# Performance work log

Measured on AMD Instinct MI355X. Metric: run time of the kernel, lower is better.

The kernel has to match this reference:

```python
import jax, jax.numpy as jnp
import numpy as np

D_MODEL = 1024
N_HEADS = 16
HEAD_DIM = D_MODEL // N_HEADS
D_FF = 4 * D_MODEL
B, T = 2, 2048
EPS = 1e-5


def setup_inputs() -> dict:
    key = jax.random.key(0)
    ks = jax.random.split(key, 12)
    s = 0.02
    x = jax.random.normal(ks[0], (B, T, D_MODEL), dtype=jnp.float32)
    # causal mask: True where attention is disallowed (masked_fill semantics)
    mask = jnp.triu(jnp.ones((T, T), dtype=bool), k=1)[None, None]
    def lin(k, out_d, in_d):
        return jax.random.normal(k, (out_d, in_d), dtype=jnp.float32) * s
    return {
        "x": x,
        "mask": mask,
        "wq_w": lin(ks[1], D_MODEL, D_MODEL), "wq_b": jnp.zeros((D_MODEL,), jnp.float32),
        "wk_w": lin(ks[2], D_MODEL, D_MODEL), "wk_b": jnp.zeros((D_MODEL,), jnp.float32),
        "wv_w": lin(ks[3], D_MODEL, D_MODEL), "wv_b": jnp.zeros((D_MODEL,), jnp.float32),
        "wo_w": lin(ks[4], D_MODEL, D_MODEL), "wo_b": jnp.zeros((D_MODEL,), jnp.float32),
        "fc1_w": lin(ks[5], D_FF, D_MODEL), "fc1_b": jnp.zeros((D_FF,), jnp.float32),
        "fc2_w": lin(ks[6], D_MODEL, D_FF), "fc2_b": jnp.zeros((D_MODEL,), jnp.float32),
        "ln1_g": jnp.ones((D_MODEL,), jnp.float32), "ln1_b": jnp.zeros((D_MODEL,), jnp.float32),
        "ln2_g": jnp.ones((D_MODEL,), jnp.float32), "ln2_b": jnp.zeros((D_MODEL,), jnp.float32),
    }


def _layer_norm(x, g, b):
    mu = jnp.mean(x, axis=-1, keepdims=True)
    var = jnp.mean(jnp.square(x - mu), axis=-1, keepdims=True)
    return (x - mu) * jax.lax.rsqrt(var + EPS) * g + b


def reference(x, mask, wq_w, wq_b, wk_w, wk_b, wv_w, wv_b, wo_w, wo_b,
              fc1_w, fc1_b, fc2_w, fc2_b, ln1_g, ln1_b, ln2_g, ln2_b):
    Bx, Tx, C = x.shape
    # --- attention sub-block (pre-norm) ---
    h = _layer_norm(x, ln1_g, ln1_b)
    q = h @ wq_w.T + wq_b
    k = h @ wk_w.T + wk_b
    v = h @ wv_w.T + wv_b
    # split heads: [B,T,C] -> [B,H,T,Dh]
    def split(t):
        return t.reshape(Bx, Tx, N_HEADS, HEAD_DIM).transpose(0, 2, 1, 3)
    q, k, v = split(q), split(k), split(v)
    scores = jnp.einsum('bhqd,bhkd->bhqk', q, k) / jnp.sqrt(jnp.float32(HEAD_DIM))
    scores = jnp.where(mask, jnp.float32(-1e9), scores)
    attn = jax.nn.softmax(scores, axis=-1)
    ctx = jnp.einsum('bhqk,bhkd->bhqd', attn, v)
    ctx = ctx.transpose(0, 2, 1, 3).reshape(Bx, Tx, C)
    x = x + (ctx @ wo_w.T + wo_b)
    # --- FFN sub-block (pre-norm) ---
    h = _layer_norm(x, ln2_g, ln2_b)
    h = jax.nn.gelu(h @ fc1_w.T + fc1_b, approximate=False)
    x = x + (h @ fc2_w.T + fc2_b)
    return x
```

## Files before the change

### kernel.cpp

```cpp
#include <hip/hip_runtime.h>
#include <stdint.h>

typedef unsigned short u16;
typedef __bf16 bf16x8 __attribute__((ext_vector_type(8)));
typedef float floatx4 __attribute__((ext_vector_type(4)));

#define AS1(p) ((__attribute__((address_space(1))) void*)(void*)(p))
#define AS3(p) ((__attribute__((address_space(3))) void*)(p))

__device__ __forceinline__ u16 f2bf(float f) {
    unsigned u;
    __builtin_memcpy(&u, &f, 4);
    u += 0x7FFF + ((u >> 16) & 1);
    return (u16)(u >> 16);
}
__device__ __forceinline__ u16 f2bf_trunc(float f) {
    unsigned u;
    __builtin_memcpy(&u, &f, 4);
    return (u16)(u >> 16);
}
__device__ __forceinline__ float exp2_fast(float x) {
    return __builtin_amdgcn_exp2f(x);
}
__device__ __forceinline__ float gelu_f(float x) {
    return 0.5f * x * (1.0f + erff(x * 0.70710678118654752f));
}

__global__ __launch_bounds__(256) void conv_w_kernel(
    const float* __restrict__ wq, const float* __restrict__ wk,
    const float* __restrict__ wv, const float* __restrict__ wo,
    const float* __restrict__ f1, const float* __restrict__ f2,
    const float* __restrict__ bq, const float* __restrict__ bk,
    const float* __restrict__ bv, float* __restrict__ qkvb,
    u16* __restrict__ W) {
    const size_t i4 = ((size_t)blockIdx.x * 256 + threadIdx.x) * 4;
    const size_t M1 = 1048576;
    const float* src;
    size_t off;
    if (i4 < M1)            { src = wq; off = i4; }
    else if (i4 < 2 * M1)   { src = wk; off = i4 - M1; }
    else if (i4 < 3 * M1)   { src = wv; off = i4 - 2 * M1; }
    else if (i4 < 4 * M1)   { src = wo; off = i4 - 3 * M1; }
    else if (i4 < 8 * M1)   { src = f1; off = i4 - 4 * M1; }
    else                    { src = f2; off = i4 - 8 * M1; }
    float4 d = *(const float4*)(src + off);
    ushort4 o;
    o.x = f2bf(d.x); o.y = f2bf(d.y); o.z = f2bf(d.z); o.w = f2bf(d.w);
    *(ushort4*)(W + i4) = o;
    if (blockIdx.x == 0) {
        for (int i = threadIdx.x; i < 1024; i += 256) {
            qkvb[i] = bq[i];
            qkvb[1024 + i] = bk[i];
            qkvb[2048 + i] = bv[i];
        }
    }
}

__global__ __launch_bounds__(64) void ln_kernel(const float* __restrict__ X,
                                                const float* __restrict__ G,
                                                const float* __restrict__ Bt,
                                                u16* __restrict__ Y) {
    const int row = blockIdx.x;
    const int lane = threadIdx.x;
    const float* xr = X + (size_t)row * 1024;
    float v[16];
    float s = 0.f;
#pragma unroll
    for (int i = 0; i < 16; ++i) { v[i] = xr[lane + i * 64]; s += v[i]; }
#pragma unroll
    for (int off = 1; off < 64; off <<= 1) s += __shfl_xor(s, off, 64);
    const float mu = s * (1.0f / 1024.0f);
    float ss = 0.f;
#pragma unroll
    for (int i = 0; i < 16; ++i) { float d = v[i] - mu; ss += d * d; }
#pragma unroll
    for (int off = 1; off < 64; off <<= 1) ss += __shfl_xor(ss, off, 64);
    const float rstd = rsqrtf(ss * (1.0f / 1024.0f) + 1e-5f);
    u16* yr = Y + (size_t)row * 1024;
#pragma unroll
    for (int i = 0; i < 16; ++i) {
        int c = lane + i * 64;
        yr[c] = f2bf((v[i] - mu) * rstd * G[c] + Bt[c]);
    }
}

template <int BM>
__global__ __launch_bounds__(256) void gemm_kernel(
    const u16* __restrict__ A, const u16* __restrict__ Bt,
    const float* __restrict__ bias, const float* __restrict__ resid,
    void* __restrict__ Cp, int M, int N, int K, int act, int c_f32) {
    constexpr int NI = BM / 32;
    __shared__ __align__(16) u16 lA[BM * 64];
    __shared__ __align__(16) u16 lB[128 * 64];
    const int tid = threadIdx.x;
    const int wave = tid >> 6, lane = tid & 63;
    const int wm = (wave >> 1) * (BM / 2), wn = (wave & 1) * 64;
    const int lr = lane & 15, lk8 = (lane >> 4) * 8;
    int bid = blockIdx.y * gridDim.x + blockIdx.x;
    { const int nwg = gridDim.x * gridDim.y;
      const int q = nwg >> 3, r = nwg & 7, xcd = bid & 7, lid = bid >> 3;
      bid = (xcd < r ? xcd * (q + 1) : r * (q + 1) + (xcd - r) * q) + lid; }
    const int m0 = (bid % gridDim.x) * BM, n0 = (bid / gridDim.x) * 128;
    const int srow = tid >> 3, scol = (tid & 7) * 8;

    floatx4 acc[NI][4];
#pragma unroll
    for (int i = 0; i < NI; ++i)
#pragma unroll
        for (int j = 0; j < 4; ++j) acc[i][j] = floatx4{0.f, 0.f, 0.f, 0.f};

    const u16* Ab = A + (size_t)m0 * K;
    const u16* Bb = Bt + (size_t)n0 * K;

    for (int k0 = 0; k0 < K; k0 += 64) {
#pragma unroll
        for (int r = 0; r < BM / 32; ++r) {
            int row = srow + r * 32;
            __builtin_amdgcn_global_load_lds(AS1(Ab + (size_t)row * K + k0 + scol),
                                             AS3(lA + row * 64 + scol), 16, 0, 0);
        }
#pragma unroll
        for (int r = 0; r < 4; ++r) {
            int row = srow + r * 32;
            __builtin_amdgcn_global_load_lds(AS1(Bb + (size_t)row * K + k0 + scol),
                                             AS3(lB + row * 64 + scol), 16, 0, 0);
        }
        __syncthreads();
#pragma unroll
        for (int kk = 0; kk < 64; kk += 32) {
            bf16x8 af[NI], bfr[4];
#pragma unroll
            for (int i = 0; i < NI; ++i)
                af[i] = *(const bf16x8*)&lA[(wm + i * 16 + lr) * 64 + kk + lk8];
#pragma unroll
            for (int j = 0; j < 4; ++j)
                bfr[j] = *(const bf16x8*)&lB[(wn + j * 16 + lr) * 64 + kk + lk8];
#pragma unroll
            for (int i = 0; i < NI; ++i)
#pragma unroll
                for (int j = 0; j < 4; ++j)
                    acc[i][j] = __builtin_amdgcn_mfma_f32_16x16x32_bf16(
                        af[i], bfr[j], acc[i][j], 0, 0, 0);
        }
        __syncthreads();
    }

    const int r0 = (lane >> 4) * 4;
#pragma unroll
    for (int i = 0; i < NI; ++i) {
#pragma unroll
        for (int j = 0; j < 4; ++j) {
            const int col = n0 + wn + j * 16 + lr;
            const float bv = bias ? bias[col] : 0.f;
#pragma unroll
            for (int r = 0; r < 4; ++r) {
                const int row = m0 + wm + i * 16 + r0 + r;
                float v2 = acc[i][j][r] + bv;
                if (act) v2 = gelu_f(v2);
                if (resid) v2 += resid[(size_t)row * N + col];
                if (c_f32)
                    ((float*)Cp)[(size_t)row * N + col] = v2;
                else
                    ((u16*)Cp)[(size_t)row * N + col] = f2bf(v2);
            }
        }
    }
}

__global__ __launch_bounds__(512, 2) void gemm256_kernel(
    const u16* __restrict__ A, const u16* __restrict__ Bt,
    const float* __restrict__ bias, u16* __restrict__ C,
    int M, int N, int K, int act) {
    extern __shared__ __align__(16) u16 smem[];
    u16* const lA = smem;
    u16* const lB = smem + 32768;
    const int tid = threadIdx.x;
    const int wave = tid >> 6, lane = tid & 63;
    const int wm = (wave >> 2) * 128;
    const int wn = (wave & 3) * 64;
    const int lr = lane & 15, lk8 = (lane >> 4) * 8;
    const int r0 = (lane >> 4) * 4;

    const int gM = M >> 8;
    int bid = blockIdx.x;
    { const int nwg = gridDim.x;
      const int q = nwg >> 3, r = nwg & 7, xcd = bid & 7, lid = bid >> 3;
      bid = (xcd < r ? xcd * (q + 1) : r * (q + 1) + (xcd - r) * q) + lid; }
    const int m0 = (bid % gM) << 8;
    const int n0 = (bid / gM) << 8;

    const int NT = K >> 6;
    const u16* const Ab = A + (size_t)m0 * K;
    const u16* const Bb = Bt + (size_t)n0 * K;

    const int srow = tid >> 3;
    const int scol = 8 * ((tid & 7) ^ (srow & 7));
    const int sdst = tid * 8;
    const int swz = (lr & 7) << 3;
    const int c0 = lk8 ^ swz;
    const int c1 = (32 + lk8) ^ swz;

    floatx4 acc[8][4];
#pragma unroll
    for (int i = 0; i < 8; ++i)
#pragma unroll
        for (int j = 0; j < 4; ++j) acc[i][j] = floatx4{0.f, 0.f, 0.f, 0.f};
    bf16x8 aF[2][4][2];
    bf16x8 bF[4][2];

#define STAGE_HT(ldsbuf, gbase, h, Tt)                                         \
    {                                                                          \
        _Pragma("unroll")                                                      \
        for (int l = 0; l < 2; ++l) {                                          \
            const u16* src = (gbase) + (size_t)((h) * 128 + l * 64 + srow) * K \
                             + (size_t)(Tt) * 64 + scol;                       \
            __builtin_amdgcn_global_load_lds(                                  \
                AS1(src), AS3((ldsbuf) + (h) * 8192 + l * 4096 + sdst), 16, 0, 0); \
        }                                                                      \
    }
#define PH_BAR() asm volatile("s_barrier" ::: "memory")
#define LGKM0()                                                                \
    do { asm volatile("s_waitcnt lgkmcnt(0)" ::: "memory");                    \
         __builtin_amdgcn_sched_barrier(0); } while (0)
#define MFMA_Q(mq, nq)                                                         \
    __builtin_amdgcn_s_setprio(1);                                             \
    _Pragma("unroll")                                                          \
    for (int i = 0; i < 4; ++i)                                                \
        _Pragma("unroll")                                                      \
        for (int j = 0; j < 2; ++j)                                            \
            _Pragma("unroll")                                                  \
            for (int kk = 0; kk < 2; ++kk)                                     \
                acc[(mq) * 4 + i][(nq) * 2 + j] =                              \
                    __builtin_amdgcn_mfma_f32_16x16x32_bf16(                   \
                        aF[mq][i][kk], bF[(nq) * 2 + j][kk],                   \
                        acc[(mq) * 4 + i][(nq) * 2 + j], 0, 0, 0);             \
    __builtin_amdgcn_s_setprio(0);

#define GROUP(P, T)                                                            \
    {                                                                          \
        u16* const lAp = lA + (P) * 16384;                                     \
        u16* const lBp = lB + (P) * 16384;                                     \
        u16* const lAn = lA + ((P) ^ 1) * 16384;                               \
        u16* const lBn = lB + ((P) ^ 1) * 16384;                               \
        (void)lAn;                                                             \
                                                                  \
        _Pragma("unroll")                                                      \
        for (int i = 0; i < 4; ++i) {                                          \
            aF[0][i][0] = *(const bf16x8*)&lAp[(wm + i * 16 + lr) * 64 + c0];  \
            aF[0][i][1] = *(const bf16x8*)&lAp[(wm + i * 16 + lr) * 64 + c1];  \
        }                                                                      \
        _Pragma("unroll")                                                      \
        for (int nf = 0; nf < 4; ++nf) {                                       \
            bF[nf][0] = *(const bf16x8*)&lBp[(wn + nf * 16 + lr) * 64 + c0];   \
            bF[nf][1] = *(const bf16x8*)&lBp[(wn + nf * 16 + lr) * 64 + c1];   \
        }                                                                      \
        if ((T) + 1 < NT) STAGE_HT(lBn, Bb, 0, (T) + 1);                       \
        PH_BAR(); LGKM0();                                                     \
        MFMA_Q(0, 0);                                                          \
        PH_BAR();                                                              \
                                                                  \
        _Pragma("unroll")                                                      \
        for (int i = 0; i < 4; ++i) {                                          \
            aF[1][i][0] = *(const bf16x8*)&lAp[(wm + 64 + i * 16 + lr) * 64 + c0]; \
            aF[1][i][1] = *(const bf16x8*)&lAp[(wm + 64 + i * 16 + lr) * 64 + c1]; \
        }                                                                      \
        if ((T) + 1 < NT) STAGE_HT(lBn, Bb, 1, (T) + 1);                       \
        PH_BAR(); LGKM0();                                                     \
        MFMA_Q(0, 1);                                                          \
        PH_BAR();                                                              \
             \
        if ((T) + 2 < NT) STAGE_HT(lAp, Ab, 0, (T) + 2);                       \
        MFMA_Q(1, 0);                                                          \
                                                                  \
        if ((T) + 2 < NT) STAGE_HT(lAp, Ab, 1, (T) + 2);                       \
        MFMA_Q(1, 1);                                                          \
        if ((T) + 2 < NT) asm volatile("s_waitcnt vmcnt(4)" ::: "memory");     \
        else              asm volatile("s_waitcnt vmcnt(0)" ::: "memory");     \
        PH_BAR();                                                              \
    }

    STAGE_HT(lA, Ab, 0, 0);
    STAGE_HT(lA, Ab, 1, 0);
    STAGE_HT(lB, Bb, 0, 0);
    STAGE_HT(lB, Bb, 1, 0);
    if (NT > 1) {
        STAGE_HT(lA + 16384, Ab, 0, 1);
        STAGE_HT(lA + 16384, Ab, 1, 1);
    }
    asm volatile("s_waitcnt vmcnt(4)" ::: "memory");
    PH_BAR();

    for (int T = 0; T < NT; T += 2) {
        GROUP(0, T);
        GROUP(1, T + 1);
    }
#undef GROUP
#undef MFMA_Q
#undef LGKM0
#undef PH_BAR
#undef STAGE_HT

#pragma unroll
    for (int mq = 0; mq < 2; ++mq)
#pragma unroll
        for (int i = 0; i < 4; ++i)
#pragma unroll
            for (int nf = 0; nf < 4; ++nf) {
                const int col = n0 + wn + nf * 16 + lr;
                const float bv = bias[col];
                floatx4 v = acc[mq * 4 + i][nf];
#pragma unroll
                for (int r = 0; r < 4; ++r) {
                    const int row = m0 + wm + mq * 64 + i * 16 + r0 + r;
                    float x = v[r] + bv;
                    if (act) x = gelu_f(x);
                    C[(size_t)row * N + col] = f2bf(x);
                }
            }
}

__global__ __launch_bounds__(256) void transp_v(const u16* __restrict__ qkv,
                                                u16* __restrict__ vT) {
    __shared__ u16 lT[64 * 64];
    const int bh = blockIdx.x, tt = blockIdx.y;
    const int b = bh >> 4, h = bh & 15;
    const int t0 = tt * 64;
    const int tid = threadIdx.x;
    const int srow = tid >> 3, scol = (tid & 7) * 8;
#pragma unroll
    for (int rr = 0; rr < 2; ++rr) {
        const int row = srow + rr * 32;
        uint4 d4 = *(const uint4*)(qkv + (size_t)(b * 2048 + t0 + row) * 3072 +
                                   2048 + h * 64 + scol);
        const u16* e = (const u16*)&d4;
#pragma unroll
        for (int t = 0; t < 8; ++t) lT[(scol + t) * 64 + row] = e[t];
    }
    __syncthreads();
#pragma unroll
    for (int rr = 0; rr < 2; ++rr) {
        const int row = srow + rr * 32;
        uint4 d4 = *(const uint4*)&lT[row * 64 + scol];
        *(uint4*)(vT + (size_t)(bh * 64 + row) * 2048 + t0 + scol) = d4;
    }
}

__global__ __launch_bounds__(256) void attn_kernel(const u16* __restrict__ qkv,
                                                   const u16* __restrict__ vT,
                                                   u16* __restrict__ O) {
    __shared__ __align__(16) u16 lK[64 * 64];
    __shared__ __align__(16) u16 lV[64 * 64];
    __shared__ __align__(16) u16 lP[4][16 * 64];
    const int tid = threadIdx.x;
    const int wave = tid >> 6, lane = tid & 63;
    const int lr = lane & 15, khi = lane >> 4, lk8 = khi * 8;
    const int p = blockIdx.x;
    const int bh = blockIdx.y;
    const int b = bh >> 4, hh = bh & 15;
    const int rb = b * 2048;
    const size_t vbase = (size_t)(bh * 64) * 2048;
    const int srow = tid >> 3, scol = (tid & 7) * 8;
    const int r0 = khi * 4;
    const int qa = 31 - p, qb = p;
    const int qa0 = qa * 64, qb0 = qb * 64;
    const float C = 0.125f * 1.44269504088896f;

    bf16x8 aqA0, aqA1, aqB0, aqB1;
    {
        const size_t qoffA = (size_t)(rb + qa0 + wave * 16 + lr) * 3072 + hh * 64;
        aqA0 = *(const bf16x8*)(qkv + qoffA + lk8);
        aqA1 = *(const bf16x8*)(qkv + qoffA + 32 + lk8);
        const size_t qoffB = (size_t)(rb + qb0 + wave * 16 + lr) * 3072 + hh * 64;
        aqB0 = *(const bf16x8*)(qkv + qoffB + lk8);
        aqB1 = *(const bf16x8*)(qkv + qoffB + 32 + lk8);
    }

    floatx4 oA[4], oB[4];
    float lA_[4], lB_[4];
#pragma unroll
    for (int r = 0; r < 4; ++r) {
        oA[r] = floatx4{0.f, 0.f, 0.f, 0.f};
        oB[r] = floatx4{0.f, 0.f, 0.f, 0.f};
        lA_[r] = 0.f; lB_[r] = 0.f;
    }

#define TILE_ROUND(aq0_, aq1_, oo_, ll_, q0_, diag_, k0_)                       \
    {                                                                           \
        float s[4][4];                                                          \
        _Pragma("unroll")                                                       \
        for (int j = 0; j < 4; ++j) {                                           \
            bf16x8 bk0 = *(const bf16x8*)&lK[(j * 16 + lr) * 64 + lk8];         \
            bf16x8 bk1 = *(const bf16x8*)&lK[(j * 16 + lr) * 64 + 32 + lk8];    \
            floatx4 t = floatx4{0.f, 0.f, 0.f, 0.f};                            \
            t = __builtin_amdgcn_mfma_f32_16x16x32_bf16(aq0_, bk0, t, 0, 0, 0); \
            t = __builtin_amdgcn_mfma_f32_16x16x32_bf16(aq1_, bk1, t, 0, 0, 0); \
            _Pragma("unroll")                                                   \
            for (int r = 0; r < 4; ++r) s[j][r] = t[r];                         \
        }                                                                       \
        if (diag_) {                                                            \
            _Pragma("unroll")                                                   \
            for (int j = 0; j < 4; ++j)                                         \
                _Pragma("unroll")                                               \
                for (int r = 0; r < 4; ++r)                                     \
                    if ((k0_) + j * 16 + lr > (q0_) + wave * 16 + r0 + r)       \
                        s[j][r] = -1e30f;                                       \
        }                                                                       \
        _Pragma("unroll")                                                       \
        for (int j = 0; j < 4; ++j)                                             \
            _Pragma("unroll")                                                   \
            for (int r = 0; r < 4; ++r) {                                       \
                float pv = exp2_fast(s[j][r] * C);                              \
                ll_[r] += pv;                                                   \
                lP[wave][(r0 + r) * 64 + j * 16 + lr] = f2bf_trunc(pv);         \
            }                                                                   \
        bf16x8 ap0 = *(const bf16x8*)&lP[wave][lr * 64 + lk8];                  \
        bf16x8 ap1 = *(const bf16x8*)&lP[wave][lr * 64 + 32 + lk8];             \
        _Pragma("unroll")                                                       \
        for (int jd = 0; jd < 4; ++jd) {                                        \
            bf16x8 bv0 = *(const bf16x8*)&lV[(jd * 16 + lr) * 64 + lk8];        \
            bf16x8 bv1 = *(const bf16x8*)&lV[(jd * 16 + lr) * 64 + 32 + lk8];   \
            oo_[jd] = __builtin_amdgcn_mfma_f32_16x16x32_bf16(ap0, bv0, oo_[jd], 0, 0, 0); \
            oo_[jd] = __builtin_amdgcn_mfma_f32_16x16x32_bf16(ap1, bv1, oo_[jd], 0, 0, 0); \
        }                                                                       \
    }

    for (int kt = 0; kt <= qa; ++kt) {
        const int k0 = kt * 64;
#pragma unroll
        for (int rr = 0; rr < 2; ++rr) {
            const int row = srow + rr * 32;
            __builtin_amdgcn_global_load_lds(
                AS1(qkv + (size_t)(rb + k0 + row) * 3072 + 1024 + hh * 64 + scol),
                AS3(lK + row * 64 + scol), 16, 0, 0);
            __builtin_amdgcn_global_load_lds(
                AS1(vT + vbase + (size_t)row * 2048 + k0 + scol),
                AS3(lV + row * 64 + scol), 16, 0, 0);
        }
        __syncthreads();

        TILE_ROUND(aqA0, aqA1, oA, lA_, qa0, kt == qa, k0);
        if (kt <= qb)
            TILE_ROUND(aqB0, aqB1, oB, lB_, qb0, kt == qb, k0);

        __syncthreads();
    }
#undef TILE_ROUND

#pragma unroll
    for (int off = 1; off < 16; off <<= 1)
#pragma unroll
        for (int r = 0; r < 4; ++r) {
            lA_[r] += __shfl_xor(lA_[r], off, 64);
            lB_[r] += __shfl_xor(lB_[r], off, 64);
        }

#pragma unroll
    for (int r = 0; r < 4; ++r) {
        const float invA = 1.0f / lA_[r];
        const float invB = 1.0f / lB_[r];
#pragma unroll
        for (int jd = 0; jd < 4; ++jd) {
            const size_t offA = (size_t)(rb + qa0 + wave * 16 + r0 + r) * 1024 +
                                hh * 64 + jd * 16 + lr;
            O[offA] = f2bf(oA[jd][r] * invA);
            const size_t offB = (size_t)(rb + qb0 + wave * 16 + r0 + r) * 1024 +
                                hh * 64 + jd * 16 + lr;
            O[offB] = f2bf(oB[jd][r] * invB);
        }
    }
}

extern "C" void kernel_launch(void* const* d_in, const int* in_sizes, int n_in,
                              void* d_out, int out_size, void* d_ws, size_t ws_size,
                              hipStream_t stream) {
    const float* x     = (const float*)d_in[0];
    const float* wq_w  = (const float*)d_in[2];
    const float* wq_b  = (const float*)d_in[3];
    const float* wk_w  = (const float*)d_in[4];
    const float* wk_b  = (const float*)d_in[5];
    const float* wv_w  = (const float*)d_in[6];
    const float* wv_b  = (const float*)d_in[7];
    const float* wo_w  = (const float*)d_in[8];
    const float* wo_b  = (const float*)d_in[9];
    const float* fc1_w = (const float*)d_in[10];
    const float* fc1_b = (const float*)d_in[11];
    const float* fc2_w = (const float*)d_in[12];
    const float* fc2_b = (const float*)d_in[13];
    const float* ln1_g = (const float*)d_in[14];
    const float* ln1_b = (const float*)d_in[15];
    const float* ln2_g = (const float*)d_in[16];
    const float* ln2_b = (const float*)d_in[17];
    float* out = (float*)d_out;

    char* ws = (char*)d_ws;
    const size_t M1 = 1048576;
    const size_t MB = 1048576;
    u16* Wc    = (u16*)ws;
    u16* wqc   = Wc;
    u16* woc   = Wc + 3 * M1;
    u16* f1c   = Wc + 4 * M1;
    u16* f2c   = Wc + 8 * M1;
    u16* h     = (u16*)(ws + 24 * MB);
    u16* ctx   = h;
    u16* qkv   = (u16*)(ws + 32 * MB);
    u16* vT    = (u16*)(ws + 56 * MB);
    u16* ffh   = (u16*)(ws + 32 * MB);
    float* x1  = (float*)(ws + 64 * MB);
    float* qkvb = x1;
    u16* h2    = h;

    const dim3 blk(256);

    static bool s_attr_done = false;
    if (!s_attr_done) {
        hipFuncSetAttribute(reinterpret_cast<const void*>(gemm256_kernel),
                            hipFuncAttributeMaxDynamicSharedMemorySize, 131072);
        s_attr_done = true;
    }

    conv_w_kernel<<<12288, 256, 0, stream>>>(wq_w, wk_w, wv_w, wo_w, fc1_w, fc2_w,
                                             wq_b, wk_b, wv_b, qkvb, Wc);
    ln_kernel<<<4096, 64, 0, stream>>>(x, ln1_g, ln1_b, h);
    gemm256_kernel<<<dim3(16 * 12), dim3(512), 131072, stream>>>(
        h, wqc, qkvb, qkv, 4096, 3072, 1024, 0);
    transp_v<<<dim3(32, 32), blk, 0, stream>>>(qkv, vT);
    attn_kernel<<<dim3(16, 32), blk, 0, stream>>>(qkv, vT, ctx);
    gemm_kernel<64><<<dim3(64, 8), blk, 0, stream>>>(
        ctx, woc, wo_b, x, x1, 4096, 1024, 1024, 0, 1);
    ln_kernel<<<4096, 64, 0, stream>>>(x1, ln2_g, ln2_b, h2);
    gemm256_kernel<<<dim3(16 * 16), dim3(512), 131072, stream>>>(
        h2, f1c, fc1_b, ffh, 4096, 4096, 1024, 1);
    gemm_kernel<64><<<dim3(64, 8), blk, 0, stream>>>(
        ffh, f2c, fc2_b, x1, out, 4096, 1024, 4096, 0, 1);
}
```

Measured before the change: 422.9 us.

## Replace generic residual GEMM with double-buffered swizzled 128x64 tile kernel

Swaps the single-buffered 64x128 gemm_kernel used for the output projection and fc2 for a new 128x64 kernel. The new kernel double-buffers LDS, prefetches the next K tile while computing the current one, and XOR-swizzles the LDS layout to cut bank conflicts. It also drops the runtime act/dtype branches in the epilogue. The tile shape changes and the XCD remapping is removed, which alters L2 reuse and occupancy (launch bounds 256,3).

```diff
diff --git a/kernel.cpp b/kernel.cpp
--- a/kernel.cpp
+++ b/kernel.cpp
@@ -84,87 +84,109 @@
     }
 }
 
-template <int BM>
-__global__ __launch_bounds__(256) void gemm_kernel(
+__global__ __launch_bounds__(256, 3) void gemm128_kernel(
     const u16* __restrict__ A, const u16* __restrict__ Bt,
     const float* __restrict__ bias, const float* __restrict__ resid,
-    void* __restrict__ Cp, int M, int N, int K, int act, int c_f32) {
-    constexpr int NI = BM / 32;
-    __shared__ __align__(16) u16 lA[BM * 64];
-    __shared__ __align__(16) u16 lB[128 * 64];
+    float* __restrict__ C, int M, int N, int K) {
+    __shared__ __align__(16) u16 lA[2 * 128 * 64];
+    __shared__ __align__(16) u16 lB[2 * 64 * 64];
     const int tid = threadIdx.x;
     const int wave = tid >> 6, lane = tid & 63;
-    const int wm = (wave >> 1) * (BM / 2), wn = (wave & 1) * 64;
+    const int wm = (wave >> 1) * 64;
+    const int wn = (wave & 1) * 32;
     const int lr = lane & 15, lk8 = (lane >> 4) * 8;
-    int bid = blockIdx.y * gridDim.x + blockIdx.x;
-    { const int nwg = gridDim.x * gridDim.y;
-      const int q = nwg >> 3, r = nwg & 7, xcd = bid & 7, lid = bid >> 3;
-      bid = (xcd < r ? xcd * (q + 1) : r * (q + 1) + (xcd - r) * q) + lid; }
-    const int m0 = (bid % gridDim.x) * BM, n0 = (bid / gridDim.x) * 128;
-    const int srow = tid >> 3, scol = (tid & 7) * 8;
-
-    floatx4 acc[NI][4];
-#pragma unroll
-    for (int i = 0; i < NI; ++i)
-#pragma unroll
-        for (int j = 0; j < 4; ++j) acc[i][j] = floatx4{0.f, 0.f, 0.f, 0.f};
-
-    const u16* Ab = A + (size_t)m0 * K;
-    const u16* Bb = Bt + (size_t)n0 * K;
-
-    for (int k0 = 0; k0 < K; k0 += 64) {
-#pragma unroll
-        for (int r = 0; r < BM / 32; ++r) {
-            int row = srow + r * 32;
-            __builtin_amdgcn_global_load_lds(AS1(Ab + (size_t)row * K + k0 + scol),
-                                             AS3(lA + row * 64 + scol), 16, 0, 0);
-        }
-#pragma unroll
-        for (int r = 0; r < 4; ++r) {
-            int row = srow + r * 32;
-            __builtin_amdgcn_global_load_lds(AS1(Bb + (size_t)row * K + k0 + scol),
-                                             AS3(lB + row * 64 + scol), 16, 0, 0);
-        }
-        __syncthreads();
-#pragma unroll
-        for (int kk = 0; kk < 64; kk += 32) {
-            bf16x8 af[NI], bfr[4];
-#pragma unroll
-            for (int i = 0; i < NI; ++i)
-                af[i] = *(const bf16x8*)&lA[(wm + i * 16 + lr) * 64 + kk + lk8];
-#pragma unroll
-            for (int j = 0; j < 4; ++j)
-                bfr[j] = *(const bf16x8*)&lB[(wn + j * 16 + lr) * 64 + kk + lk8];
-#pragma unroll
-            for (int i = 0; i < NI; ++i)
-#pragma unroll
-                for (int j = 0; j < 4; ++j)
-                    acc[i][j] = __builtin_amdgcn_mfma_f32_16x16x32_bf16(
-                        af[i], bfr[j], acc[i][j], 0, 0, 0);
-        }
-        __syncthreads();
-    }
-
     const int r0 = (lane >> 4) * 4;
-#pragma unroll
-    for (int i = 0; i < NI; ++i) {
-#pragma unroll
-        for (int j = 0; j < 4; ++j) {
+    const int m0 = blockIdx.x * 128, n0 = blockIdx.y * 64;
+    const int NT = K >> 6;
+    const u16* const Ab = A + (size_t)m0 * K;
+    const u16* const Bb = Bt + (size_t)n0 * K;
+
+    const int srow = tid >> 3;
+    const int scol = 8 * ((tid & 7) ^ (srow & 7));
+    const int sdst = tid * 8;
+    const int swz = (lr & 7) << 3;
+    const int c0 = lk8 ^ swz;
+    const int c1 = (32 + lk8) ^ swz;
+
+    floatx4 acc[4][2];
+#pragma unroll
+    for (int i = 0; i < 4; ++i)
+#pragma unroll
+        for (int j = 0; j < 2; ++j) acc[i][j] = floatx4{0.f, 0.f, 0.f, 0.f};
+    bf16x8 aF[4][2], bF[2][2];
+
+#define STAGE128(Pb, Tt)                                                       \
+    {                                                                          \
+        _Pragma("unroll")                                                      \
+        for (int l = 0; l < 4; ++l) {                                          \
+            const u16* srcA = Ab + (size_t)(l * 32 + srow) * K +               \
+                              (size_t)(Tt) * 64 + scol;                        \
+            __builtin_amdgcn_global_load_lds(                                  \
+                AS1(srcA), AS3(lA + (Pb) * 8192 + l * 2048 + sdst), 16, 0, 0); \
+        }                                                                      \
+        _Pragma("unroll")                                                      \
+        for (int l = 0; l < 2; ++l) {                                          \
+            const u16* srcB = Bb + (size_t)(l * 32 + srow) * K +               \
+                              (size_t)(Tt) * 64 + scol;                        \
+            __builtin_amdgcn_global_load_lds(                                  \
+                AS1(srcB), AS3(lB + (Pb) * 4096 + l * 2048 + sdst), 16, 0, 0); \
+        }                                                                      \
+    }
+#define GROUP128(P, T)                                                         \
+    {                                                                          \
+        if ((T) + 1 < NT) {                                                    \
+            STAGE128((P) ^ 1, (T) + 1);                                        \
+            asm volatile("s_waitcnt vmcnt(6)" ::: "memory");                   \
+        } else {                                                               \
+            asm volatile("s_waitcnt vmcnt(0)" ::: "memory");                   \
+        }                                                                      \
+        asm volatile("s_barrier" ::: "memory");                                \
+        _Pragma("unroll")                                                      \
+        for (int i = 0; i < 4; ++i) {                                          \
+            aF[i][0] = *(const bf16x8*)&lA[(P) * 8192 + (wm + i * 16 + lr) * 64 + c0]; \
+            aF[i][1] = *(const bf16x8*)&lA[(P) * 8192 + (wm + i * 16 + lr) * 64 + c1]; \
+        }                                                                      \
+        _Pragma("unroll")                                                      \
+        for (int j = 0; j < 2; ++j) {                                          \
+            bF[j][0] = *(const bf16x8*)&lB[(P) * 4096 + (wn + j * 16 + lr) * 64 + c0]; \
+            bF[j][1] = *(const bf16x8*)&lB[(P) * 4096 + (wn + j * 16 + lr) * 64 + c1]; \
+        }                                                                      \
+        asm volatile("s_waitcnt lgkmcnt(0)" ::: "memory");                     \
+        __builtin_amdgcn_sched_barrier(0);                                     \
+        __builtin_amdgcn_s_setprio(1);                                         \
+        _Pragma("unroll")                                                      \
+        for (int i = 0; i < 4; ++i)                                            \
+            _Pragma("unroll")                                                  \
+            for (int j = 0; j < 2; ++j)                                        \
+                _Pragma("unroll")                                              \
+                for (int kk = 0; kk < 2; ++kk)                                 \
+                    acc[i][j] = __builtin_amdgcn_mfma_f32_16x16x32_bf16(       \
+                        aF[i][kk], bF[j][kk], acc[i][j], 0, 0, 0);             \
+        __builtin_amdgcn_s_setprio(0);                                         \
+        asm volatile("s_barrier" ::: "memory");                                \
+    }
+
+    STAGE128(0, 0);
+    for (int T = 0; T < NT; T += 2) {
+        GROUP128(0, T);
+        GROUP128(1, T + 1);
+    }
+#undef GROUP128
+#undef STAGE128
+
+#pragma unroll
+    for (int i = 0; i < 4; ++i)
+#pragma unroll
+        for (int j = 0; j < 2; ++j) {
             const int col = n0 + wn + j * 16 + lr;
-            const float bv = bias ? bias[col] : 0.f;
+            const float bv = bias[col];
 #pragma unroll
             for (int r = 0; r < 4; ++r) {
                 const int row = m0 + wm + i * 16 + r0 + r;
-                float v2 = acc[i][j][r] + bv;
-                if (act) v2 = gelu_f(v2);
-                if (resid) v2 += resid[(size_t)row * N + col];
-                if (c_f32)
-                    ((float*)Cp)[(size_t)row * N + col] = v2;
-                else
-                    ((u16*)Cp)[(size_t)row * N + col] = f2bf(v2);
+                C[(size_t)row * N + col] =
+                    acc[i][j][r] + bv + resid[(size_t)row * N + col];
             }
         }
-    }
 }
 
 __global__ __launch_bounds__(512, 2) void gemm256_kernel(
@@ -240,9 +262,7 @@
     {                                                                          \
         u16* const lAp = lA + (P) * 16384;                                     \
         u16* const lBp = lB + (P) * 16384;                                     \
-        u16* const lAn = lA + ((P) ^ 1) * 16384;                               \
         u16* const lBn = lB + ((P) ^ 1) * 16384;                               \
-        (void)lAn;                                                             \
                                                                   \
         _Pragma("unroll")                                                      \
         for (int i = 0; i < 4; ++i) {                                          \
@@ -525,11 +545,11 @@
         h, wqc, qkvb, qkv, 4096, 3072, 1024, 0);
     transp_v<<<dim3(32, 32), blk, 0, stream>>>(qkv, vT);
     attn_kernel<<<dim3(16, 32), blk, 0, stream>>>(qkv, vT, ctx);
-    gemm_kernel<64><<<dim3(64, 8), blk, 0, stream>>>(
-        ctx, woc, wo_b, x, x1, 4096, 1024, 1024, 0, 1);
+    gemm128_kernel<<<dim3(32, 16), blk, 0, stream>>>(
+        ctx, woc, wo_b, x, x1, 4096, 1024, 1024);
     ln_kernel<<<4096, 64, 0, stream>>>(x1, ln2_g, ln2_b, h2);
     gemm256_kernel<<<dim3(16 * 16), dim3(512), 131072, stream>>>(
         h2, f1c, fc1_b, ffh, 4096, 4096, 1024, 1);
-    gemm_kernel<64><<<dim3(64, 8), blk, 0, stream>>>(
-        ffh, f2c, fc2_b, x1, out, 4096, 1024, 4096, 0, 1);
-}
+    gemm128_kernel<<<dim3(32, 16), blk, 0, stream>>>(
+        ffh, f2c, fc2_b, x1, out, 4096, 1024, 4096);
+}
```

Result: faster. 371.3 us (-12.2%).
